# Performance work log

Hardware: AMD Instinct MI355X
Metric: run time of the kernel (lower is better)

## Reference

```python
import jax, jax.numpy as jnp
import numpy as np

HEADS = 16
DIM_HEAD = 64
SCALE = DIM_HEAD ** -0.5
MASK_VALUE = -jnp.finfo(jnp.float32).max


def setup_inputs() -> dict:
    key = jax.random.key(0)
    ks = jax.random.split(key, 6)
    b, n, dim = 2, 2048, 1024
    mem_len = 2048
    inner = HEADS * DIM_HEAD  # 1024
    return {
        "x": jax.random.normal(ks[0], (b, n, dim), jnp.float32),
        "mem_k": jax.random.normal(ks[1], (b, mem_len, inner), jnp.float32),
        "mem_v": jax.random.normal(ks[2], (b, mem_len, inner), jnp.float32),
        "pos_bias": jax.random.normal(ks[3], (HEADS, n, mem_len + n), jnp.float32) * 0.02,
        "Wq": jax.random.normal(ks[4], (dim, inner), jnp.float32) * (dim ** -0.5),
        "Wkv": jax.random.normal(ks[5], (dim, 2 * inner), jnp.float32) * (dim ** -0.5),
    }


def reference(x, mem_k, mem_v, pos_bias, Wq, Wkv):
    b, n, _ = x.shape
    # projections (note: original module returns before applying to_out)
    q = (x @ Wq) * SCALE                      # [b, n, h*d]
    k, v = jnp.split(x @ Wkv, 2, axis=-1)     # each [b, n, h*d]
    k = jnp.concatenate((mem_k, k), axis=1)   # [b, j, h*d]
    v = jnp.concatenate((mem_v, v), axis=1)

    def split_heads(t):
        return t.reshape(t.shape[0], t.shape[1], HEADS, DIM_HEAD).transpose(0, 2, 1, 3)

    q, k, v = map(split_heads, (q, k, v))     # [b, h, i/j, d]
    sim = jnp.einsum('bhid,bhjd->bhij', q, k)
    sim = sim + pos_bias[None]                # broadcast over batch
    i, j = sim.shape[-2:]
    # causal mask: triu with offset j - i + 1 is masked out
    causal_mask = jnp.triu(jnp.ones((i, j), dtype=bool), k=j - i + 1)
    sim = jnp.where(causal_mask[None, None], MASK_VALUE, sim)
    attn = jax.nn.softmax(sim, axis=-1)
    out = jnp.einsum('bhij,bhjd->bhid', attn, v)     # [b, h, i, d]
    out = out.transpose(0, 2, 1, 3).reshape(b, n, HEADS * DIM_HEAD)
    return out
```

## Files before the change

kernel.cpp:

```cpp
#include <hip/hip_runtime.h>
#include <hip/hip_bf16.h>
#include <cstdint>

#define B_     2
#define N_     2048
#define DIM_   1024
#define H_     16
#define DH_    64
#define MEM_   2048
#define JT_    4096
#define INNER_ 1024
#define SCALE_ 0.125f

typedef float f32x4 __attribute__((ext_vector_type(4)));
typedef short s16x8 __attribute__((ext_vector_type(8)));
typedef short s16x4 __attribute__((ext_vector_type(4)));

__device__ __forceinline__ short bf16_of(float f) {
    __hip_bfloat16 h = __float2bfloat16(f);
    return *(short*)&h;
}

__device__ __forceinline__ void gload16(const void* g, short* l) {
    __builtin_amdgcn_global_load_lds(
        (const __attribute__((address_space(1))) unsigned int*)g,
        (__attribute__((address_space(3))) unsigned int*)l, 16, 0, 0);
}

__global__ __launch_bounds__(256) void cast_x(
    const float* __restrict__ x, short* __restrict__ xb)
{
    const int total4 = B_ * N_ * DIM_ / 4;
    for (int idx = blockIdx.x * blockDim.x + threadIdx.x; idx < total4;
         idx += gridDim.x * blockDim.x) {
        float4 v = ((const float4*)x)[idx];
        s16x4 o;
        o[0] = bf16_of(v.x); o[1] = bf16_of(v.y);
        o[2] = bf16_of(v.z); o[3] = bf16_of(v.w);
        *(s16x4*)&xb[idx * 4] = o;
    }
}

__global__ __launch_bounds__(256) void cast_w(
    const float* __restrict__ Wq, const float* __restrict__ Wkv,
    short* __restrict__ Wt)
{
    const int kt = blockIdx.x;
    const int nt = blockIdx.y;
    __shared__ float tile[64][65];
    const int t = threadIdx.x;
    const int r = t >> 2, s4 = (t & 3) * 16;

    const int n0 = nt * 64;
    const float* src;
    int ldn, nc0;
    if (n0 < 1024) { src = Wq;  ldn = 1024; nc0 = n0; }
    else           { src = Wkv; ldn = 2048; nc0 = n0 - 1024; }
    const float scale = (n0 < 1024) ? SCALE_ : 1.0f;

#pragma unroll
    for (int kq = 0; kq < 4; ++kq) {
        float4 v = *(const float4*)&src[(size_t)(kt * 64 + r) * ldn + nc0 + s4 + kq * 4];
        tile[s4 + kq * 4 + 0][r] = v.x;
        tile[s4 + kq * 4 + 1][r] = v.y;
        tile[s4 + kq * 4 + 2][r] = v.z;
        tile[s4 + kq * 4 + 3][r] = v.w;
    }
    __syncthreads();
    short ov[16];
#pragma unroll
    for (int e = 0; e < 16; ++e) ov[e] = bf16_of(tile[r][s4 + e] * scale);
    short* dst = &Wt[(size_t)(n0 + r) * 1024 + kt * 64 + s4];
    *(s16x8*)&dst[0] = *(s16x8*)&ov[0];
    *(s16x8*)&dst[8] = *(s16x8*)&ov[8];
}

#define PLDC 152

__global__ __launch_bounds__(256) void mfma_proj(
    const short* __restrict__ Wt, const short* __restrict__ xb,
    short* __restrict__ qbuf, short* __restrict__ kbuf, short* __restrict__ vtbuf)
{
    const int bc = blockIdx.x;
    const int bi = blockIdx.y;
    const int tid = threadIdx.x;
    const int w = tid >> 6, lane = tid & 63, g = lane >> 4, li = lane & 15;
    const int wr = w >> 1, wc = w & 1;

    __shared__ short smem[128 * PLDC];
    short* A_lds = smem;
    short* B_lds = smem + 8192;

    f32x4 acc[4][4];
#pragma unroll
    for (int m = 0; m < 4; ++m)
#pragma unroll
        for (int n = 0; n < 4; ++n) acc[m][n] = f32x4{0.f, 0.f, 0.f, 0.f};

    const size_t arow0 = (size_t)bc * 128;
    const size_t brow0 = (size_t)bi * 128;

    for (int t = 0; t < 16; ++t) {
        __syncthreads();
#pragma unroll
        for (int u = 0; u < 4; ++u) {
            const int c = (w * 4 + u) * 64 + lane;
            const int row = c >> 3, q = c & 7;
            const int qs = q ^ (row & 7);
            gload16(&Wt[(arow0 + row) * 1024 + t * 64 + qs * 8],
                    &A_lds[(w * 4 + u) * 512 + lane * 8]);
            gload16(&xb[(brow0 + row) * 1024 + t * 64 + qs * 8],
                    &B_lds[(w * 4 + u) * 512 + lane * 8]);
        }
        __syncthreads();
#pragma unroll
        for (int kc = 0; kc < 2; ++kc) {
            s16x8 af[4], bf[4];
#pragma unroll
            for (int mt = 0; mt < 4; ++mt) {
                const int row = wr * 64 + mt * 16 + li;
                af[mt] = *(const s16x8*)&A_lds[row * 64 + ((kc * 4 + g) ^ (row & 7)) * 8];
            }
#pragma unroll
            for (int nt = 0; nt < 4; ++nt) {
                const int row = wc * 64 + nt * 16 + li;
                bf[nt] = *(const s16x8*)&B_lds[row * 64 + ((kc * 4 + g) ^ (row & 7)) * 8];
            }
#pragma unroll
            for (int mt = 0; mt < 4; ++mt)
#pragma unroll
                for (int nt = 0; nt < 4; ++nt)
                    acc[mt][nt] = __builtin_amdgcn_mfma_f32_16x16x32_bf16(af[mt], bf[nt], acc[mt][nt], 0, 0, 0);
        }
    }

    __syncthreads();
    const int c0 = bc * 128;
    const int i0g = bi * 128;
    const int b = i0g >> 11;
    const int ii0 = i0g & 2047;

    if (c0 < 2048) {
#pragma unroll
        for (int mt = 0; mt < 4; ++mt)
#pragma unroll
            for (int nt = 0; nt < 4; ++nt) {
                const int i_l = wc * 64 + nt * 16 + li;
                const int c_l = wr * 64 + mt * 16 + g * 4;
                s16x4 v4;
                v4[0] = bf16_of(acc[mt][nt][0]);
                v4[1] = bf16_of(acc[mt][nt][1]);
                v4[2] = bf16_of(acc[mt][nt][2]);
                v4[3] = bf16_of(acc[mt][nt][3]);
                *(s16x4*)&smem[i_l * PLDC + c_l] = v4;
            }
        __syncthreads();
        const bool isq = (c0 < 1024);
#pragma unroll
        for (int u = 0; u < 8; ++u) {
            const int ch = tid + u * 256;
            const int i_l = ch >> 4, seg = ch & 15;
            s16x8 v = *(const s16x8*)&smem[i_l * PLDC + seg * 8];
            const int cg = c0 + seg * 8;
            const int h = (cg >> 6) & 15;
            const int d = cg & 63;
            if (isq)
                *(s16x8*)&qbuf[(((size_t)(b * H_ + h)) * N_ + ii0 + i_l) * DH_ + d] = v;
            else
                *(s16x8*)&kbuf[(((size_t)(b * H_ + h)) * JT_ + MEM_ + ii0 + i_l) * DH_ + d] = v;
        }
    } else {
#pragma unroll
        for (int mt = 0; mt < 4; ++mt)
#pragma unroll
            for (int nt = 0; nt < 4; ++nt) {
                const int i_l = wc * 64 + nt * 16 + li;
                const int c_b = wr * 64 + mt * 16 + g * 4;
#pragma unroll
                for (int r = 0; r < 4; ++r)
                    smem[(c_b + r) * PLDC + i_l] = bf16_of(acc[mt][nt][r]);
            }
        __syncthreads();
#pragma unroll
        for (int u = 0; u < 8; ++u) {
            const int ch = tid + u * 256;
            const int c_l = ch >> 4, seg = ch & 15;
            s16x8 v = *(const s16x8*)&smem[c_l * PLDC + seg * 8];
            const int cv = c0 + c_l - 2048;
            const int h = cv >> 6, d = cv & 63;
            *(s16x8*)&vtbuf[(((size_t)(b * H_ + h)) * DH_ + d) * JT_ + MEM_ + ii0 + seg * 8] = v;
        }
    }
}

__global__ __launch_bounds__(256) void prep_mem(
    const float* __restrict__ mem_k, const float* __restrict__ mem_v,
    short* __restrict__ kbuf, short* __restrict__ vtbuf)
{
    const int jt = blockIdx.x, h = blockIdx.y;
    const int b = blockIdx.z & 1, task = blockIdx.z >> 1;
    const int j0 = jt * 64;
    const int t = threadIdx.x;
    const int r = t >> 2, s4 = (t & 3) * 16;
    const size_t bh = (size_t)(b * H_ + h);

    if (task == 0) {
        short ov[16];
#pragma unroll
        for (int k = 0; k < 4; ++k) {
            float4 v = *(const float4*)&mem_k[((size_t)(b * MEM_ + j0 + r)) * INNER_ + h * DH_ + s4 + k * 4];
            ov[k * 4 + 0] = bf16_of(v.x);
            ov[k * 4 + 1] = bf16_of(v.y);
            ov[k * 4 + 2] = bf16_of(v.z);
            ov[k * 4 + 3] = bf16_of(v.w);
        }
        short* dst = &kbuf[(bh * JT_ + j0 + r) * DH_ + s4];
        *(s16x8*)&dst[0] = *(s16x8*)&ov[0];
        *(s16x8*)&dst[8] = *(s16x8*)&ov[8];
    } else {
        __shared__ float tile[64][65];
#pragma unroll
        for (int k = 0; k < 4; ++k) {
            float4 v = *(const float4*)&mem_v[((size_t)(b * MEM_ + j0 + r)) * INNER_ + h * DH_ + s4 + k * 4];
            tile[s4 + k * 4 + 0][r] = v.x;
            tile[s4 + k * 4 + 1][r] = v.y;
            tile[s4 + k * 4 + 2][r] = v.z;
            tile[s4 + k * 4 + 3][r] = v.w;
        }
        __syncthreads();
        short ov[16];
#pragma unroll
        for (int e = 0; e < 16; ++e) ov[e] = bf16_of(tile[r][s4 + e]);
        short* dst = &vtbuf[(bh * DH_ + r) * JT_ + j0 + s4];
        *(s16x8*)&dst[0] = *(s16x8*)&ov[0];
        *(s16x8*)&dst[8] = *(s16x8*)&ov[8];
    }
}

__global__ __launch_bounds__(256, 4) void attn_flash(
    const short* __restrict__ qbuf, const short* __restrict__ kbuf,
    const short* __restrict__ vtbuf, const float* __restrict__ pos_bias,
    float* __restrict__ out)
{
    const int lid = blockIdx.x;
    const int h   = (lid & 7) | (((lid >> 3) & 1) << 3);
    const int b   = (lid >> 4) & 1;
    const int zql = (lid >> 5) & 15;
    const int hi  = lid >> 9;
    const int zq  = hi ? (31 - zql) : zql;
    const int i0  = zq * 64;

    const int tid = threadIdx.x;
    const int w = tid >> 6, lane = tid & 63, g = lane >> 4, li = lane & 15;

    __shared__ short K_lds[2][64 * 64];
    __shared__ short VT_lds[2][64 * 64];
    __shared__ short P_lds[4][16 * 64];

    const size_t bh = (size_t)(b * H_ + h);
    const short* kg  = kbuf  + bh * (size_t)JT_ * DH_;
    const short* vtg = vtbuf + bh * (size_t)DH_ * JT_;
    const float* pb  = pos_bias + (size_t)h * N_ * JT_;

    const int qw = i0 + w * 16;

    s16x8 aq[2];
#pragma unroll
    for (int kc = 0; kc < 2; ++kc)
        aq[kc] = *(const s16x8*)&qbuf[(bh * N_ + qw + li) * DH_ + kc * 32 + g * 8];

    f32x4 o[4];
    float m_run = -3.0e38f, l_run = 0.f;
#pragma unroll
    for (int dt = 0; dt < 4; ++dt) o[dt] = f32x4{0.f, 0.f, 0.f, 0.f};

    const int ntiles = 33 + zq;

    #define STAGE(bufi, j0s)                                                   \
    {                                                                          \
        _Pragma("unroll")                                                      \
        for (int u = 0; u < 2; ++u) {                                          \
            const int c = u * 256 + tid;                                       \
            const int row = c >> 3, q = c & 7;                                 \
            const int qs = q ^ (row & 7);                                      \
            gload16(&kg[(size_t)((j0s) + row) * DH_ + qs * 8],                 \
                    &K_lds[bufi][c * 8]);                                      \
            gload16(&vtg[(size_t)row * JT_ + (j0s) + qs * 8],                  \
                    &VT_lds[bufi][c * 8]);                                     \
        }                                                                      \
    }

    f32x4 bnext[4];
    #define LOADB(j0s)                                                         \
    {                                                                          \
        _Pragma("unroll")                                                      \
        for (int nt = 0; nt < 4; ++nt)                                         \
            bnext[nt] = *(const f32x4*)&pb[(size_t)(qw + li) * JT_ + (j0s) + nt * 16 + g * 4]; \
    }

    STAGE(0, 0);
    LOADB(0);
    __syncthreads();

    for (int t = 0; t < ntiles; ++t) {
        const int cur = t & 1;
        const int j0 = t * 64;
        const bool more = (t + 1 < ntiles);

        if (more) STAGE(cur ^ 1, j0 + 64);

        f32x4 sacc[4];
#pragma unroll
        for (int nt = 0; nt < 4; ++nt) sacc[nt] = bnext[nt];

        if (more) LOADB(j0 + 64);

        __builtin_amdgcn_s_setprio(1);
#pragma unroll
        for (int kc = 0; kc < 2; ++kc)
#pragma unroll
            for (int nt = 0; nt < 4; ++nt) {
                s16x8 bk = *(const s16x8*)&K_lds[cur][(nt * 16 + li) * 64 + ((kc * 4 + g) ^ (li & 7)) * 8];
                sacc[nt] = __builtin_amdgcn_mfma_f32_16x16x32_bf16(bk, aq[kc], sacc[nt], 0, 0, 0);
            }
        __builtin_amdgcn_s_setprio(0);

        const int q = qw + li;
        if (j0 + 63 > MEM_ + qw) {
#pragma unroll
            for (int nt = 0; nt < 4; ++nt)
#pragma unroll
                for (int r = 0; r < 4; ++r) {
                    const int jg = j0 + nt * 16 + g * 4 + r;
                    if (jg > MEM_ + q) sacc[nt][r] = -1e30f;
                }
        }

        float t0 = fmaxf(fmaxf(sacc[0][0], sacc[0][1]), fmaxf(sacc[0][2], sacc[0][3]));
        float t1 = fmaxf(fmaxf(sacc[1][0], sacc[1][1]), fmaxf(sacc[1][2], sacc[1][3]));
        float t2 = fmaxf(fmaxf(sacc[2][0], sacc[2][1]), fmaxf(sacc[2][2], sacc[2][3]));
        float t3 = fmaxf(fmaxf(sacc[3][0], sacc[3][1]), fmaxf(sacc[3][2], sacc[3][3]));
        float tm = fmaxf(fmaxf(t0, t1), fmaxf(t2, t3));
        tm = fmaxf(tm, __shfl_xor(tm, 16));
        tm = fmaxf(tm, __shfl_xor(tm, 32));
        const float m_new = fmaxf(m_run, tm);
        const float sc = __expf(m_run - m_new);
        m_run = m_new;

#pragma unroll
        for (int nt = 0; nt < 4; ++nt)
#pragma unroll
            for (int r = 0; r < 4; ++r)
                sacc[nt][r] = __expf(sacc[nt][r] - m_new);

        float s0 = (sacc[0][0] + sacc[0][1]) + (sacc[0][2] + sacc[0][3]);
        float s1 = (sacc[1][0] + sacc[1][1]) + (sacc[1][2] + sacc[1][3]);
        float s2 = (sacc[2][0] + sacc[2][1]) + (sacc[2][2] + sacc[2][3]);
        float s3 = (sacc[3][0] + sacc[3][1]) + (sacc[3][2] + sacc[3][3]);
        float ts = (s0 + s1) + (s2 + s3);
        ts += __shfl_xor(ts, 16);
        ts += __shfl_xor(ts, 32);
        l_run = l_run * sc + ts;
#pragma unroll
        for (int dt = 0; dt < 4; ++dt) o[dt] *= sc;

#pragma unroll
        for (int nt = 0; nt < 4; ++nt) {
            const int sl = nt * 4 + g;
            const int gi = (sl >> 1) ^ (li & 7);
            s16x4 pk;
            pk[0] = bf16_of(sacc[nt][0]);
            pk[1] = bf16_of(sacc[nt][1]);
            pk[2] = bf16_of(sacc[nt][2]);
            pk[3] = bf16_of(sacc[nt][3]);
            *(s16x4*)&P_lds[w][li * 64 + gi * 8 + (sl & 1) * 4] = pk;
        }

        __builtin_amdgcn_s_setprio(1);
#pragma unroll
        for (int kc = 0; kc < 2; ++kc) {
            const int gir = (kc * 4 + g) ^ (li & 7);
            s16x8 pf = *(const s16x8*)&P_lds[w][li * 64 + gir * 8];
#pragma unroll
            for (int dt = 0; dt < 4; ++dt) {
                s16x8 bv = *(const s16x8*)&VT_lds[cur][(dt * 16 + li) * 64 + ((kc * 4 + g) ^ (li & 7)) * 8];
                o[dt] = __builtin_amdgcn_mfma_f32_16x16x32_bf16(bv, pf, o[dt], 0, 0, 0);
            }
        }
        __builtin_amdgcn_s_setprio(0);

        __syncthreads();
    }
    #undef STAGE
    #undef LOADB

    {
        const float rinv = 1.0f / l_run;
        const int q = qw + li;
#pragma unroll
        for (int dt = 0; dt < 4; ++dt) {
            f32x4 ov = o[dt] * rinv;
            *(f32x4*)&out[((size_t)(b * N_ + q)) * INNER_ + h * DH_ + dt * 16 + g * 4] = ov;
        }
    }
}

extern "C" void kernel_launch(void* const* d_in, const int* in_sizes, int n_in,
                              void* d_out, int out_size, void* d_ws, size_t ws_size,
                              hipStream_t stream)
{
    const float* x        = (const float*)d_in[0];
    const float* mem_k    = (const float*)d_in[1];
    const float* mem_v    = (const float*)d_in[2];
    const float* pos_bias = (const float*)d_in[3];
    const float* Wq       = (const float*)d_in[4];
    const float* Wkv      = (const float*)d_in[5];
    float* out = (float*)d_out;

    char* ws = (char*)d_ws;
    short* qbuf  = (short*)(ws);
    short* kbuf  = (short*)(ws + (8u << 20));
    short* vtbuf = (short*)(ws + (24u << 20));
    short* xb    = (short*)(ws + (40u << 20));
    short* Wt    = (short*)(ws + (48u << 20));

    cast_x<<<2048, 256, 0, stream>>>(x, xb);
    cast_w<<<dim3(16, 48), 256, 0, stream>>>(Wq, Wkv, Wt);
    prep_mem<<<dim3(32, H_, 4), 256, 0, stream>>>(mem_k, mem_v, kbuf, vtbuf);

    mfma_proj<<<dim3(24, 32), 256, 0, stream>>>(Wt, xb, qbuf, kbuf, vtbuf);

    attn_flash<<<1024, 256, 0, stream>>>(qbuf, kbuf, vtbuf, pos_bias, out);
}
```

Baseline: 228.0 us.

## Halve attention KV tile to 32 keys to raise occupancy to five blocks

Shrinks the key tile from 64 to 32 columns, which halves the K/VT shared-memory buffers, shrinks the padded P buffer, and halves the score and bias registers. The launch bound moves from 4 to 5 blocks per SM so more waves can hide latency. The cost is twice as many loop iterations, each with its own barrier, online-softmax rescale and cross-lane reductions, so fixed per-tile overhead grows. The V-transpose LDS swizzle and P layout are reworked to fit the narrower tile.

```diff
diff --git a/kernel.cpp b/kernel.cpp
--- a/kernel.cpp
+++ b/kernel.cpp
@@ -237,7 +237,7 @@
     }
 }
 
-__global__ __launch_bounds__(256, 4) void attn_flash(
+__global__ __launch_bounds__(256, 5) void attn_flash(
     const short* __restrict__ qbuf, const short* __restrict__ kbuf,
     const short* __restrict__ vtbuf, const float* __restrict__ pos_bias,
     float* __restrict__ out)
@@ -253,9 +253,9 @@
     const int tid = threadIdx.x;
     const int w = tid >> 6, lane = tid & 63, g = lane >> 4, li = lane & 15;
 
-    __shared__ short K_lds[2][64 * 64];
-    __shared__ short VT_lds[2][64 * 64];
-    __shared__ short P_lds[4][16 * 64];
+    __shared__ short K_lds[2][32 * 64];
+    __shared__ short VT_lds[2][64 * 32];
+    __shared__ short P_lds[4][16 * 40];
 
     const size_t bh = (size_t)(b * H_ + h);
     const short* kg  = kbuf  + bh * (size_t)JT_ * DH_;
@@ -274,27 +274,25 @@
 #pragma unroll
     for (int dt = 0; dt < 4; ++dt) o[dt] = f32x4{0.f, 0.f, 0.f, 0.f};
 
-    const int ntiles = 33 + zq;
+    const int ntiles = 66 + 2 * zq;
 
     #define STAGE(bufi, j0s)                                                   \
     {                                                                          \
-        _Pragma("unroll")                                                      \
-        for (int u = 0; u < 2; ++u) {                                          \
-            const int c = u * 256 + tid;                                       \
-            const int row = c >> 3, q = c & 7;                                 \
-            const int qs = q ^ (row & 7);                                      \
-            gload16(&kg[(size_t)((j0s) + row) * DH_ + qs * 8],                 \
-                    &K_lds[bufi][c * 8]);                                      \
-            gload16(&vtg[(size_t)row * JT_ + (j0s) + qs * 8],                  \
-                    &VT_lds[bufi][c * 8]);                                     \
-        }                                                                      \
-    }
-
-    f32x4 bnext[4];
+        const int rowk = tid >> 3, qk = tid & 7;                               \
+        const int qks = qk ^ (rowk & 7);                                       \
+        gload16(&kg[(size_t)((j0s) + rowk) * DH_ + qks * 8],                   \
+                &K_lds[bufi][tid * 8]);                                        \
+        const int rv = tid >> 2, qv = tid & 3;                                 \
+        const int qvs = qv ^ ((rv >> 1) & 3);                                  \
+        gload16(&vtg[(size_t)rv * JT_ + (j0s) + qvs * 8],                      \
+                &VT_lds[bufi][tid * 8]);                                       \
+    }
+
+    f32x4 bnext[2];
     #define LOADB(j0s)                                                         \
     {                                                                          \
         _Pragma("unroll")                                                      \
-        for (int nt = 0; nt < 4; ++nt)                                         \
+        for (int nt = 0; nt < 2; ++nt)                                         \
             bnext[nt] = *(const f32x4*)&pb[(size_t)(qw + li) * JT_ + (j0s) + nt * 16 + g * 4]; \
     }
 
@@ -304,31 +302,31 @@
 
     for (int t = 0; t < ntiles; ++t) {
         const int cur = t & 1;
-        const int j0 = t * 64;
+        const int j0 = t * 32;
         const bool more = (t + 1 < ntiles);
 
-        if (more) STAGE(cur ^ 1, j0 + 64);
-
-        f32x4 sacc[4];
-#pragma unroll
-        for (int nt = 0; nt < 4; ++nt) sacc[nt] = bnext[nt];
-
-        if (more) LOADB(j0 + 64);
+        if (more) STAGE(cur ^ 1, j0 + 32);
+
+        f32x4 sacc[2];
+#pragma unroll
+        for (int nt = 0; nt < 2; ++nt) sacc[nt] = bnext[nt];
+
+        if (more) LOADB(j0 + 32);
 
         __builtin_amdgcn_s_setprio(1);
 #pragma unroll
         for (int kc = 0; kc < 2; ++kc)
 #pragma unroll
-            for (int nt = 0; nt < 4; ++nt) {
+            for (int nt = 0; nt < 2; ++nt) {
                 s16x8 bk = *(const s16x8*)&K_lds[cur][(nt * 16 + li) * 64 + ((kc * 4 + g) ^ (li & 7)) * 8];
                 sacc[nt] = __builtin_amdgcn_mfma_f32_16x16x32_bf16(bk, aq[kc], sacc[nt], 0, 0, 0);
             }
         __builtin_amdgcn_s_setprio(0);
 
         const int q = qw + li;
-        if (j0 + 63 > MEM_ + qw) {
-#pragma unroll
-            for (int nt = 0; nt < 4; ++nt)
+        if (j0 + 31 > MEM_ + qw) {
+#pragma unroll
+            for (int nt = 0; nt < 2; ++nt)
 #pragma unroll
                 for (int r = 0; r < 4; ++r) {
                     const int jg = j0 + nt * 16 + g * 4 + r;
@@ -338,9 +336,7 @@
 
         float t0 = fmaxf(fmaxf(sacc[0][0], sacc[0][1]), fmaxf(sacc[0][2], sacc[0][3]));
         float t1 = fmaxf(fmaxf(sacc[1][0], sacc[1][1]), fmaxf(sacc[1][2], sacc[1][3]));
-        float t2 = fmaxf(fmaxf(sacc[2][0], sacc[2][1]), fmaxf(sacc[2][2], sacc[2][3]));
-        float t3 = fmaxf(fmaxf(sacc[3][0], sacc[3][1]), fmaxf(sacc[3][2], sacc[3][3]));
-        float tm = fmaxf(fmaxf(t0, t1), fmaxf(t2, t3));
+        float tm = fmaxf(t0, t1);
         tm = fmaxf(tm, __shfl_xor(tm, 16));
         tm = fmaxf(tm, __shfl_xor(tm, 32));
         const float m_new = fmaxf(m_run, tm);
@@ -348,16 +344,14 @@
         m_run = m_new;
 
 #pragma unroll
-        for (int nt = 0; nt < 4; ++nt)
+        for (int nt = 0; nt < 2; ++nt)
 #pragma unroll
             for (int r = 0; r < 4; ++r)
                 sacc[nt][r] = __expf(sacc[nt][r] - m_new);
 
         float s0 = (sacc[0][0] + sacc[0][1]) + (sacc[0][2] + sacc[0][3]);
         float s1 = (sacc[1][0] + sacc[1][1]) + (sacc[1][2] + sacc[1][3]);
-        float s2 = (sacc[2][0] + sacc[2][1]) + (sacc[2][2] + sacc[2][3]);
-        float s3 = (sacc[3][0] + sacc[3][1]) + (sacc[3][2] + sacc[3][3]);
-        float ts = (s0 + s1) + (s2 + s3);
+        float ts = s0 + s1;
         ts += __shfl_xor(ts, 16);
         ts += __shfl_xor(ts, 32);
         l_run = l_run * sc + ts;
@@ -365,25 +359,22 @@
         for (int dt = 0; dt < 4; ++dt) o[dt] *= sc;
 
 #pragma unroll
-        for (int nt = 0; nt < 4; ++nt) {
-            const int sl = nt * 4 + g;
-            const int gi = (sl >> 1) ^ (li & 7);
+        for (int nt = 0; nt < 2; ++nt) {
             s16x4 pk;
             pk[0] = bf16_of(sacc[nt][0]);
             pk[1] = bf16_of(sacc[nt][1]);
             pk[2] = bf16_of(sacc[nt][2]);
             pk[3] = bf16_of(sacc[nt][3]);
-            *(s16x4*)&P_lds[w][li * 64 + gi * 8 + (sl & 1) * 4] = pk;
+            *(s16x4*)&P_lds[w][li * 40 + nt * 16 + g * 4] = pk;
         }
 
         __builtin_amdgcn_s_setprio(1);
-#pragma unroll
-        for (int kc = 0; kc < 2; ++kc) {
-            const int gir = (kc * 4 + g) ^ (li & 7);
-            s16x8 pf = *(const s16x8*)&P_lds[w][li * 64 + gir * 8];
+        {
+            s16x8 pf = *(const s16x8*)&P_lds[w][li * 40 + g * 8];
 #pragma unroll
             for (int dt = 0; dt < 4; ++dt) {
-                s16x8 bv = *(const s16x8*)&VT_lds[cur][(dt * 16 + li) * 64 + ((kc * 4 + g) ^ (li & 7)) * 8];
+                const int row = dt * 16 + li;
+                s16x8 bv = *(const s16x8*)&VT_lds[cur][row * 32 + (g ^ ((row >> 1) & 3)) * 8];
                 o[dt] = __builtin_amdgcn_mfma_f32_16x16x32_bf16(bv, pf, o[dt], 0, 0, 0);
             }
         }
```

After: 265.9 us. 1.17x slower.
